# Optimization experiments

Hardware: AMD Instinct MI355X
Metric: run time of the kernel (lower is better)

The kernel has to match this reference:

```python
import jax, jax.numpy as jnp
import numpy as np

N_ITER, N_TAPS, N_DELAY, N_SRC = 2, 4, 1, 4
EPS = 1e-3
TINY = 1e-20
BATCH, N_CHAN, N_FREQ, N_FRAMES = 2, 6, 320, 500


def mag_sq(x):
    return x.real ** 2 + x.imag ** 2


def divide(num, denom, eps):
    return num / jnp.maximum(denom, eps)


def make_xbar(X, n_taps, n_delay):
    # X: (..., c, f, n) -> X_bar: (..., c, f, t, n); tap t is X delayed by n_delay + t
    n = X.shape[-1]
    pad = [(0, 0)] * (X.ndim - 1)
    taps = [jnp.pad(X, pad + [(n_delay + t, 0)])[..., :n] for t in range(n_taps)]
    return jnp.stack(taps, axis=-2)


def background_update(W, H, C_XX, C_XbarX, eps=1e-5):
    # recompute J from W, H and input covariances (ridge-loaded solve)
    n_src = W.shape[-3]
    A1 = jnp.einsum('...sfc,...cfd->...fsd', W, C_XX)
    A2 = jnp.einsum('...sfdt,...dtfc->...fsc', H, C_XbarX)
    Am = A1 + A2
    mat = Am[..., :n_src]
    load = jnp.abs(jnp.diagonal(mat, axis1=-2, axis2=-1)).sum(axis=-1)[..., None, None]
    load = jnp.maximum(load * eps, eps) * jnp.eye(n_src, dtype=mat.dtype)
    load = jax.lax.stop_gradient(load)
    J_H = jnp.linalg.solve(mat + load, Am[..., n_src:])
    return jnp.moveaxis(J_H.conj(), -1, -3)  # (..., n_bak, f, n_src)


def iss_type1(src, Y, w, eps):
    n = Y.shape[-1]
    Ys = Y[..., src, :, :]
    vn = jnp.einsum('...cfn,...cfn,...fn->...cf', w, Y, Ys.conj()) / n
    vd = jnp.einsum('...cfn,...fn->...cf', w, mag_sq(Ys)) / n
    v = divide(vn, vd, eps)
    vs = 1.0 - 1.0 / jnp.sqrt(jnp.maximum(vd[..., src, :], eps))
    return v.at[..., src, :].set(vs.astype(v.dtype))


def iss_type2(Y, Zs, w, eps):
    vn = jnp.einsum('...cfn,...cfn,...fn->...cf', w, Y, Zs.conj())
    vd = jnp.einsum('...cfn,...fn->...cf', w, mag_sq(Zs))
    return divide(vn, vd, eps)


def iss_type3(src, tap, Y, X_bar, w, eps):
    Xst = X_bar[..., src, :, tap, :]
    vn = jnp.einsum('...cfn,...cfn,...fn->...cf', w, Y, Xst.conj())
    vd = jnp.einsum('...cfn,...fn->...cf', w, mag_sq(Xst))
    return divide(vn, vd, eps)


def mat_up1(W, H, A, v, src, eps):
    Wn = W - jnp.einsum('...cf,...fd->...cfd', v, W[..., src, :, :])
    Hn = H - jnp.einsum('...cf,...fdt->...cfdt', v, H[..., src, :, :, :])
    u = jnp.einsum('...sfc,...cf->...sf', A[..., :v.shape[-2]], v)
    u = u / (1.0 - v[..., src:src + 1, :] + eps)
    return Wn, Hn, A.at[..., src].add(u)


def mat_up2(W, J, A, v, g, eps):
    n_src = W.shape[-3]
    v2 = v[..., :n_src, :] + jnp.einsum('...sfc,...cf->...sf', W[..., n_src:], v[..., n_src:, :])
    W1 = W[..., :n_src] - jnp.einsum('...cf,...fd->...cfd', v[..., :n_src, :], g)
    Wn = jnp.concatenate([W1, W[..., n_src:]], axis=-1)
    Jn = J - jnp.einsum('...cf,...fd->...cfd', v[..., n_src:, :], g)
    Av = jnp.einsum('...sfc,...cf->...sf', A[..., :v2.shape[-2]], v2)
    gA = jnp.einsum('...fs,...sfc->...fc', g, A[..., :g.shape[-1], :, :])
    denom = 1.0 - jnp.einsum('...cf,...fc->...f', v2, gA)
    mul = denom.conj() / (mag_sq(denom) + eps)
    An = A + jnp.einsum('...sf,...fc->...sfc', Av, gA * mul[..., None])
    return Wn, Jn, An


def bak_update_vector(p, d, g, eps):
    gdg = jnp.sum(mag_sq(g) / (d + eps), axis=-2)
    gdp = jnp.sum(g.conj() * p / (d + eps), axis=-2)
    b = 1.0 - gdp
    b1 = mag_sq(b)
    a = b1 * gdg + TINY
    beta = (-b1 + jnp.sqrt(b1 ** 2 + 4.0 * a)) / (2.0 * a)
    ell1 = beta * b
    ell2 = (1.0 / jnp.sqrt(eps + gdg)).astype(ell1.dtype)
    ell = jnp.where(b1 > eps ** 2, ell1, ell2)
    return (p - ell[..., None, :] * g) / (d + eps)


def bak_update(bak, Y, Z, X, W, J, A, w, eps):
    n_src, n_freq, n_frames = Y.shape[-3:]
    n_chan = X.shape[-3]
    Zs = Z[..., bak, :, :] + X[..., n_src + bak, :, :]
    norm = 1.0 / n_frames
    ones = jnp.ones(w.shape[:-3] + (n_chan - n_src, n_freq, n_frames), w.dtype)
    wz = jnp.concatenate([w, ones], axis=-3)
    YZ = jnp.concatenate([Y, Z], axis=-3)
    p = jnp.einsum('...cfn,...cfn,...fn->...cf', YZ, wz, Zs.conj()) * norm
    d = jnp.einsum('...cfn,...fn->...cf', wz, mag_sq(Zs)) * norm
    A2 = jnp.concatenate([A, jnp.einsum('...sfc,...cfd->...sfd', A, W[..., n_src:])], axis=-1)
    g = jnp.einsum('...fs,...sfc->...cf', J[..., bak, :, :], A2).conj()
    v = bak_update_vector(p, d, g, eps)
    YZ = YZ - jnp.einsum('...cf,...fn->...cfn', v, Zs)
    return v, YZ[..., :n_src, :, :], YZ[..., n_src:, :, :]


def iss_updates(Y, X, X_bar, W, H, A, w, J, Z, eps):
    n_src = Y.shape[-3]
    n_chan = X.shape[-3]
    n_taps = X_bar.shape[-2]
    n_bak = n_chan - n_src
    # 1) background rows (structured type-2 updates)
    for bak in range(n_bak):
        v, Y, Z = bak_update(bak, Y, Z, X, W, J, A, w, eps)
        g = J[..., bak, :, :]
        W, J, A = mat_up2(W, J, A, v, g, eps)
    # 2) source directions (type 1)
    for src in range(n_src):
        v = iss_type1(src, Y, w, eps)
        Y = Y - jnp.einsum('...cf,...fn->...cfn', v, Y[..., src, :, :])
        W, H, A = mat_up1(W, H, A, v, src, eps)
    # 3) background directions (type 2)
    for bak in range(n_bak):
        v = iss_type2(Y, Z[..., bak, :, :], w, eps)
        Y = Y - jnp.einsum('...cf,...fn->...cfn', v, Z[..., bak, :, :])
        W = W.at[..., :n_src].add(-jnp.einsum('...cf,...fd->...cfd', v, J[..., bak, :, :]))
        W = W.at[..., n_src + bak].add(v)
    if n_bak > 0:
        # keep A consistent: A = inv(W1 + W2 J) per frequency
        Binv = W[..., :n_src] + jnp.einsum('...sfc,...cfd->...sfd', W[..., n_src:], J)
        A = jnp.moveaxis(jnp.linalg.inv(jnp.moveaxis(Binv, -2, -3)), -3, -2)
    # 4) dereverberation taps (type 3)
    for src in range(n_chan):
        for tap in range(n_taps):
            v = iss_type3(src, tap, Y, X_bar, w, eps)
            Y = Y - jnp.einsum('...cf,...fn->...cfn', v, X_bar[..., src, :, tap, :])
            H = H.at[..., src, tap].add(v)
    return Y, Z, W, H, J, A


def _forward(X):
    batch = X.shape[:-3]
    n_chan, n_freq, n_frames = X.shape[-3:]
    n_src = N_SRC
    X_bar = make_xbar(X, N_TAPS, N_DELAY)
    W = jnp.broadcast_to(jnp.eye(n_src, n_chan, dtype=X.dtype)[:, None, :], batch + (n_src, n_freq, n_chan))
    H = jnp.zeros(batch + (n_src, n_freq, n_chan, N_TAPS), X.dtype)
    A = jnp.broadcast_to(jnp.eye(n_src, dtype=X.dtype)[:, None, :], batch + (n_src, n_freq, n_src))
    # initialize background demixing J from input second-order statistics
    C_XX = jnp.einsum('...cfn,...dfn->...cfd', X, X.conj()) / n_frames
    C_XbarX = jnp.einsum('...dftn,...cfn->...dtfc', X_bar, X.conj()) / n_frames
    J = background_update(W, H, C_XX, C_XbarX)
    Y = X[..., :n_src, :, :]
    Z = jnp.einsum('...cfd,...dfn->...cfn', J, X[..., :n_src, :, :]) - X[..., n_src:, :, :]
    for _ in range(N_ITER):
        # Gauss (time-varying) source-model weights, shared across frequencies
        w = 1.0 / jnp.maximum(jnp.mean(mag_sq(Y), axis=-2, keepdims=True), EPS)
        w = jnp.broadcast_to(w, Y.shape)
        Y, Z, W, H, J, A = iss_updates(Y, X, X_bar, W, H, A, w, J, Z, EPS)
    return Y


def setup_inputs():
    key = jax.random.key(0)
    k1, k2 = jax.random.split(key)
    shape = (BATCH, N_CHAN, N_FREQ, N_FRAMES)
    return {"X_real": jax.random.normal(k1, shape, jnp.float32),
            "X_imag": jax.random.normal(k2, shape, jnp.float32)}


def reference(X_real, X_imag):
    X = jax.lax.complex(X_real, X_imag)
    return _forward(X)
```

## Files before the change

kernel.cpp:

```cpp
#include <hip/hip_runtime.h>

#define NFR 500
#define NFQ 320
#define NB  2
#define NC  6
#define NS  4
#define NBK 2
#define NT  4
#define NDLY 1
#define EPSF 1e-3f
#define TINYF 1e-20f

#define NP   512
#define XPAD 8
#define XLEN (XPAD + NP)
#define NCH  8
#define FPC  (NFQ / NCH)

typedef float f2 __attribute__((ext_vector_type(2)));

__device__ __forceinline__ f2 mk2(float r, float i){ f2 t; t.x = r; t.y = i; return t; }
__device__ __forceinline__ f2 cmul(f2 a, f2 b){ return a.xx*b + a.yy*mk2(-b.y, b.x); }
__device__ __forceinline__ f2 cmulc(f2 a, f2 b){ return b.xx*a + b.yy*mk2(a.y, -a.x); }
__device__ __forceinline__ f2 conjc(f2 a){ return mk2(a.x, -a.y); }
__device__ __forceinline__ float cmag2(f2 a){ return a.x*a.x + a.y*a.y; }
__device__ __forceinline__ f2 cinv(f2 a){ float m = a.x*a.x + a.y*a.y; return mk2(a.x/m, -a.y/m); }

#define DPPF(x, ctrl) __int_as_float(__builtin_amdgcn_mov_dpp(__float_as_int(x), (ctrl), 0xF, 0xF, true))
__device__ __forceinline__ float wred64(float x){
  x += DPPF(x, 0x111);
  x += DPPF(x, 0x112);
  x += DPPF(x, 0x114);
  x += DPPF(x, 0x118);
  x += DPPF(x, 0x142);
  x += DPPF(x, 0x143);
  return __int_as_float(__builtin_amdgcn_readlane(__float_as_int(x), 63));
}

__global__ __launch_bounds__(512) void k_wpartX(const float* __restrict__ Xr,
                                                const float* __restrict__ Xi,
                                                float* __restrict__ wacc)
{
  const int bs = blockIdx.x / NCH;
  const int ch = blockIdx.x % NCH;
  const int n  = threadIdx.x;
  if (n >= NFR) return;
  const int b = bs / NS, s = bs % NS;
  const size_t rowb = ((size_t)(b*NC + s)*NFQ)*NFR;
  float acc = 0.f;
  for (int ff = 0; ff < FPC; ++ff) {
    size_t idx = rowb + (size_t)(ch*FPC + ff)*NFR + n;
    float xr = Xr[idx], xi = Xi[idx];
    acc += xr*xr + xi*xi;
  }
  wacc[((size_t)(ch*NB*NS + bs))*NFR + n] = acc;
}

__global__ __launch_bounds__(512) void k_wpart(const f2* __restrict__ Yg,
                                               float* __restrict__ wacc)
{
  const int bs = blockIdx.x / NCH;
  const int ch = blockIdx.x % NCH;
  const int n  = threadIdx.x;
  if (n >= NFR) return;
  const f2* row = Yg + (size_t)bs*NFQ*NFR;
  f2 acc2 = mk2(0.f,0.f);
  for (int ff = 0; ff < FPC; ++ff) {
    f2 y = row[(size_t)(ch*FPC + ff)*NFR + n];
    acc2 += y*y;
  }
  wacc[((size_t)(ch*NB*NS + bs))*NFR + n] = acc2.x + acc2.y;
}

__global__ __launch_bounds__(256, 3) void k_iter(
  const float* __restrict__ Xr, const float* __restrict__ Xi,
  f2* __restrict__ Yg, f2* __restrict__ Zg,
  f2* __restrict__ Wg, f2* __restrict__ Jg, f2* __restrict__ Ag,
  const float* __restrict__ wacc, float* __restrict__ outR,
  const int first, const int last)
{
  __shared__ f2 sXp[NC][XLEN];
  __shared__ f2 sZ[NBK][NP];
  __shared__ f2 sS[NP];
  __shared__ f2 sW[NS][NC];
  __shared__ f2 sJ[NBK][NS];
  __shared__ f2 sA[NS][NS];
  __shared__ f2 sB[NS][2*NS];
  __shared__ f2 sv[NC], sg[NC], sgo[NS];
  __shared__ float sd[NC];
  __shared__ f2 sp[NC];
  __shared__ f2 sAv[NS], sgA[NS], sWsrc[NC];

  const int bf = blockIdx.x;
  const int b = bf / NFQ, f = bf % NFQ;
  const int tid = threadIdx.x, wv = tid >> 6, lane = tid & 63;

  f2 yreg[8];
  float wreg[8];

  for (int c = 0; c < NC; ++c) {
    const size_t base = ((size_t)(b*NC + c)*NFQ + f)*NFR;
    for (int j = tid; j < XLEN; j += 256) {
      int n = j - XPAD;
      sXp[c][j] = (n >= 0 && n < NFR) ? mk2(Xr[base+n], Xi[base+n]) : mk2(0.f,0.f);
    }
  }

  if (first) {
    __syncthreads();
    for (int p = wv; p < NS*NC; p += 4) {
      int s = p / NC, d = p % NC;
      f2 ar2 = mk2(0.f,0.f), ai2 = mk2(0.f,0.f);
#pragma unroll
      for (int i = 0; i < 8; ++i) {
        int n = lane + 64*i;
        f2 xs = sXp[s][XPAD+n], xd = sXp[d][XPAD+n];
        ar2 += xs * xd;
        ai2 += xs.yx * mk2(xd.x, -xd.y);
      }
      float ar = wred64(ar2.x + ar2.y), ai = wred64(ai2.x + ai2.y);
      if (lane == 0) sB[s][d] = mk2(ar*(1.f/NFR), ai*(1.f/NFR));
    }
    if (tid >= 192 && tid < 192 + NS*NC) {
      int t = tid - 192; sW[t/NC][t%NC] = (t/NC == t%NC) ? mk2(1.f,0.f) : mk2(0.f,0.f);
    } else if (tid >= 224 && tid < 224 + NS*NS) {
      int t = tid - 224; sA[t/NS][t%NS] = (t/NS == t%NS) ? mk2(1.f,0.f) : mk2(0.f,0.f);
    }
    __syncthreads();
    if (tid == 0) {
      f2 M[NS][NC];
      for (int s = 0; s < NS; ++s)
        for (int d = 0; d < NC; ++d) M[s][d] = sB[s][d];
      float dsum = 0.f;
      for (int s = 0; s < NS; ++s) dsum += sqrtf(cmag2(M[s][s]));
      float load = fmaxf(dsum*1e-5f, 1e-5f);
      for (int s = 0; s < NS; ++s) M[s][s].x += load;
      for (int col = 0; col < NS; ++col) {
        int piv = col; float best = cmag2(M[col][col]);
        for (int r = col+1; r < NS; ++r) { float m = cmag2(M[r][col]); if (m > best){best=m; piv=r;} }
        if (piv != col) for (int k = 0; k < NC; ++k) { f2 t=M[col][k]; M[col][k]=M[piv][k]; M[piv][k]=t; }
        f2 ip = cinv(M[col][col]);
        for (int k = col; k < NC; ++k) M[col][k] = cmul(M[col][k], ip);
        for (int r = 0; r < NS; ++r) if (r != col) {
          f2 fac = M[r][col];
          for (int k = col; k < NC; ++k) M[r][k] -= cmul(fac, M[col][k]);
        }
      }
      for (int k = 0; k < NBK; ++k)
        for (int s = 0; s < NS; ++s) sJ[k][s] = conjc(M[s][NS+k]);
    }
    __syncthreads();
    for (int n = tid; n < NP; n += 256) {
      f2 x0 = sXp[0][XPAD+n], x1 = sXp[1][XPAD+n], x2 = sXp[2][XPAD+n], x3 = sXp[3][XPAD+n];
      f2 a0 = -sXp[NS+0][XPAD+n];
      a0 += cmul(sJ[0][0], x0); a0 += cmul(sJ[0][1], x1);
      a0 += cmul(sJ[0][2], x2); a0 += cmul(sJ[0][3], x3);
      f2 a1 = -sXp[NS+1][XPAD+n];
      a1 += cmul(sJ[1][0], x0); a1 += cmul(sJ[1][1], x1);
      a1 += cmul(sJ[1][2], x2); a1 += cmul(sJ[1][3], x3);
      sZ[0][n] = a0; sZ[1][n] = a1;
    }
    {
      const int bs = b*NS + wv;
#pragma unroll
      for (int i = 0; i < 8; ++i) {
        int n = lane + 64*i;
        yreg[i] = sXp[wv][XPAD+n];
        if (n < NFR) {
          float a = 0.f;
#pragma unroll
          for (int cc = 0; cc < NCH; ++cc) a += wacc[((size_t)(cc*NB*NS + bs))*NFR + n];
          wreg[i] = 1.0f / fmaxf(a * (1.0f/(float)NFQ), EPSF);
        } else wreg[i] = 0.f;
      }
    }
    __syncthreads();
  } else {
    for (int k = 0; k < NBK; ++k) {
      const size_t zb = ((size_t)(b*NBK + k)*NFQ + f)*NFR;
      for (int n = tid; n < NP; n += 256) sZ[k][n] = (n < NFR) ? Zg[zb+n] : mk2(0.f,0.f);
    }
    {
      const size_t yb = ((size_t)(b*NS + wv)*NFQ + f)*NFR;
      const int bs = b*NS + wv;
#pragma unroll
      for (int i = 0; i < 8; ++i) {
        int n = lane + 64*i;
        if (n < NFR) {
          yreg[i] = Yg[yb+n];
          float a = 0.f;
#pragma unroll
          for (int cc = 0; cc < NCH; ++cc) a += wacc[((size_t)(cc*NB*NS + bs))*NFR + n];
          wreg[i] = 1.0f / fmaxf(a * (1.0f/(float)NFQ), EPSF);
        } else { yreg[i] = mk2(0.f,0.f); wreg[i] = 0.f; }
      }
    }
    if (tid < NS*NC) sW[tid/NC][tid%NC] = Wg[((size_t)(b*NS + tid/NC)*NFQ + f)*NC + tid%NC];
    else if (tid < NS*NC + NBK*NS) { int t=tid-NS*NC; sJ[t/NS][t%NS] = Jg[((size_t)(b*NBK+t/NS)*NFQ+f)*NS + t%NS]; }
    else if (tid < NS*NC + NBK*NS + NS*NS) { int t=tid-NS*NC-NBK*NS; sA[t/NS][t%NS] = Ag[((size_t)(b*NS+t/NS)*NFQ+f)*NS + t%NS]; }
    __syncthreads();
  }

  f2 vloc[NC];

  for (int bak = 0; bak < NBK; ++bak) {
    if (bak > 0 && tid < 16) {
      int s = tid >> 2, c = tid & 3;
      f2 v2[NS];
#pragma unroll
      for (int t = 0; t < NS; ++t)
        v2[t] = vloc[t] + cmul(sW[t][NS+0], vloc[NS+0]) + cmul(sW[t][NS+1], vloc[NS+1]);
      f2 den = mk2(1.f,0.f);
#pragma unroll
      for (int cc = 0; cc < NS; ++cc) den -= cmul(v2[cc], sgA[cc]);
      float m2 = cmag2(den) + EPSF;
      f2 mul = mk2(den.x/m2, -den.y/m2);
      sA[s][c] += cmul(sAv[s], cmul(sgA[c], mul));
    }
    __syncthreads();

    f2 zs[8];
    {
      f2 pr2 = mk2(0.f,0.f), pi2 = mk2(0.f,0.f), dd2 = mk2(0.f,0.f);
#pragma unroll
      for (int i = 0; i < 8; ++i) {
        int n = lane+64*i;
        zs[i] = sZ[bak][n] + sXp[NS+bak][XPAD+n];
        f2 wy = wreg[i]*yreg[i];
        pr2 += wy * zs[i];
        pi2 += wy.yx * mk2(zs[i].x, -zs[i].y);
        dd2 += (wreg[i]*zs[i]) * zs[i];
      }
      float pr = wred64(pr2.x+pr2.y), pi = wred64(pi2.x+pi2.y), dd = wred64(dd2.x+dd2.y);
      if (lane == 0) { sp[wv] = mk2(pr*(1.f/NFR), pi*(1.f/NFR)); sd[wv] = dd*(1.f/NFR); }
      if (wv < NBK) {
        f2 qr2 = mk2(0.f,0.f), qi2 = mk2(0.f,0.f), qd2 = mk2(0.f,0.f);
#pragma unroll
        for (int i = 0; i < 8; ++i) {
          f2 y = sZ[wv][lane+64*i];
          qr2 += y * zs[i];
          qi2 += y.yx * mk2(zs[i].x, -zs[i].y);
          qd2 += zs[i]*zs[i];
        }
        float qr = wred64(qr2.x+qr2.y), qi = wred64(qi2.x+qi2.y), qd = wred64(qd2.x+qd2.y);
        if (lane == 0) { sp[NS+wv] = mk2(qr*(1.f/NFR), qi*(1.f/NFR)); sd[NS+wv] = qd*(1.f/NFR); }
      }
    }
    if (tid < NC) {
      int c = tid; f2 acc = mk2(0.f,0.f);
      for (int s = 0; s < NS; ++s) {
        f2 a2;
        if (c < NS) a2 = sA[s][c];
        else {
          a2 = mk2(0.f,0.f);
          for (int k = 0; k < NS; ++k) a2 += cmul(sA[s][k], sW[k][c]);
        }
        acc += cmul(sJ[bak][s], a2);
      }
      sg[c] = conjc(acc);
    } else if (tid >= 8 && tid < 8+NS) {
      sgo[tid-8] = sJ[bak][tid-8];
    }
    __syncthreads();

    {
      float gdg = 0.f; f2 gdp = mk2(0.f,0.f);
#pragma unroll
      for (int c = 0; c < NC; ++c) {
        f2 gc = sg[c]; float id = 1.0f/(sd[c] + EPSF);
        gdg += cmag2(gc) * id;
        gdp += id * cmulc(sp[c], gc);
      }
      f2 bb = mk2(1.0f - gdp.x, -gdp.y);
      float b1 = cmag2(bb);
      float a = b1*gdg + TINYF;
      float beta = (-b1 + sqrtf(b1*b1 + 4.0f*a)) / (2.0f*a);
      f2 ell = (b1 > EPSF*EPSF) ? (beta*bb) : mk2(1.0f/sqrtf(EPSF + gdg), 0.f);
#pragma unroll
      for (int c = 0; c < NC; ++c)
        vloc[c] = (1.0f/(sd[c] + EPSF)) * (sp[c] - cmul(ell, sg[c]));
    }
    {
      f2 vc = vloc[wv];
#pragma unroll
      for (int i = 0; i < 8; ++i) yreg[i] -= cmul(vc, zs[i]);
      if (wv < NBK) {
        f2 v2c = vloc[NS+wv];
#pragma unroll
        for (int i = 0; i < 8; ++i) sZ[wv][lane+64*i] -= cmul(v2c, zs[i]);
      }
    }
    __syncthreads();

    if (tid < NS) {
      f2 v2[NS];
#pragma unroll
      for (int t = 0; t < NS; ++t)
        v2[t] = vloc[t] + cmul(sW[t][NS+0], vloc[NS+0]) + cmul(sW[t][NS+1], vloc[NS+1]);
      f2 acc = mk2(0.f,0.f);
#pragma unroll
      for (int c = 0; c < NS; ++c) acc += cmul(sA[tid][c], v2[c]);
      sAv[tid] = acc;
    } else if (tid < 2*NS) {
      int c = tid - NS; f2 acc = mk2(0.f,0.f);
#pragma unroll
      for (int s = 0; s < NS; ++s) acc += cmul(sgo[s], sA[s][c]);
      sgA[c] = acc;
    } else if (tid < 2*NS + 16) {
      int idx = tid - 2*NS; int cc = idx >> 2, d = idx & 3;
      sW[cc][d] -= cmul(vloc[cc], sgo[d]);
    } else if (tid < 2*NS + 16 + 8) {
      int idx = tid - 2*NS - 16; int k = idx >> 2, d = idx & 3;
      sJ[k][d] -= cmul(vloc[NS+k], sgo[d]);
    }
    __syncthreads();
  }

  for (int src = 0; src < NS; ++src) {
    if (wv == src) {
#pragma unroll
      for (int i = 0; i < 8; ++i) sS[lane+64*i] = yreg[i];
    }
    if (tid < NC) sWsrc[tid] = sW[src][tid];
    if (src == 0) {
      if (tid < 16) {
        int s = tid >> 2, c = tid & 3;
        f2 v2[NS];
#pragma unroll
        for (int t = 0; t < NS; ++t)
          v2[t] = vloc[t] + cmul(sW[t][NS+0], vloc[NS+0]) + cmul(sW[t][NS+1], vloc[NS+1]);
        f2 den = mk2(1.f,0.f);
#pragma unroll
        for (int cc = 0; cc < NS; ++cc) den -= cmul(v2[cc], sgA[cc]);
        float m2 = cmag2(den) + EPSF;
        f2 mul = mk2(den.x/m2, -den.y/m2);
        sA[s][c] += cmul(sAv[s], cmul(sgA[c], mul));
      }
    } else if (tid >= 8 && tid < 8+NS) {
      int r = tid - 8, prev = src - 1;
      f2 acc = mk2(0.f,0.f);
#pragma unroll
      for (int c = 0; c < NS; ++c) acc += cmul(sA[r][c], sv[c]);
      float den = 1.0f - sv[prev].x + EPSF;
      sA[r][prev] += (1.0f/den) * acc;
    }
    __syncthreads();

    {
      f2 ys[8];
      f2 nr2 = mk2(0.f,0.f), ni2 = mk2(0.f,0.f), dd2 = mk2(0.f,0.f);
#pragma unroll
      for (int i = 0; i < 8; ++i) {
        ys[i] = sS[lane+64*i];
        f2 wy = wreg[i]*yreg[i];
        nr2 += wy * ys[i];
        ni2 += wy.yx * mk2(ys[i].x, -ys[i].y);
        dd2 += (wreg[i]*ys[i]) * ys[i];
      }
      float nr = wred64(nr2.x+nr2.y)*(1.f/NFR);
      float ni = wred64(ni2.x+ni2.y)*(1.f/NFR);
      float dd = wred64(dd2.x+dd2.y)*(1.f/NFR);
      f2 vc;
      if (wv == src) vc = mk2(1.0f - 1.0f/sqrtf(fmaxf(dd, EPSF)), 0.f);
      else           vc = (1.0f/fmaxf(dd, EPSF)) * mk2(nr, ni);
      if (lane == 0) sv[wv] = vc;
#pragma unroll
      for (int i = 0; i < 8; ++i) yreg[i] -= cmul(vc, ys[i]);
      if (lane < NC) sW[wv][lane] -= cmul(vc, sWsrc[lane]);
    }
    __syncthreads();
  }

  {
    f2 pr0=mk2(0,0), pi0=mk2(0,0), dd0=mk2(0,0);
    f2 pr1=mk2(0,0), pi1=mk2(0,0), dd1=mk2(0,0);
    f2 crr=mk2(0,0), cri=mk2(0,0);
    f2 z0c[8], z1c[8];
#pragma unroll
    for (int i = 0; i < 8; ++i) {
      f2 z0 = sZ[0][lane+64*i], z1 = sZ[1][lane+64*i];
      z0c[i] = z0; z1c[i] = z1;
      f2 wy = wreg[i]*yreg[i];
      f2 wz0 = wreg[i]*z0;
      pr0 += wy * z0;  pi0 += wy.yx * mk2(z0.x, -z0.y);  dd0 += wz0 * z0;
      pr1 += wy * z1;  pi1 += wy.yx * mk2(z1.x, -z1.y);  dd1 += (wreg[i]*z1) * z1;
      crr += wz0 * z1; cri += wz0.yx * mk2(z1.x, -z1.y);
    }
    float P0r = wred64(pr0.x+pr0.y), P0i = wred64(pi0.x+pi0.y), D0 = wred64(dd0.x+dd0.y);
    float P1r = wred64(pr1.x+pr1.y), P1i = wred64(pi1.x+pi1.y), D1 = wred64(dd1.x+dd1.y);
    float Rr  = wred64(crr.x+crr.y), Ri  = wred64(cri.x+cri.y);
    f2 v0 = (1.0f/fmaxf(D0, EPSF)) * mk2(P0r, P0i);
    f2 P1c = mk2(P1r, P1i) - cmul(v0, mk2(Rr, Ri));
    f2 v1 = (1.0f/fmaxf(D1, EPSF)) * P1c;
#pragma unroll
    for (int i = 0; i < 8; ++i) yreg[i] -= cmul(v0, z0c[i]) + cmul(v1, z1c[i]);
    if (lane < NS) sW[wv][lane] -= cmul(v0, sJ[0][lane]) + cmul(v1, sJ[1][lane]);
    else if (lane == NS)   sW[wv][NS+0] += v0;
    else if (lane == NS+1) sW[wv][NS+1] += v1;
  }
  __syncthreads();

  if (!last) {
    if (tid < 16) {
      int s = tid >> 2, d = tid & 3;
      f2 acc = sW[s][d];
      acc += cmul(sW[s][NS+0], sJ[0][d]);
      acc += cmul(sW[s][NS+1], sJ[1][d]);
      sB[s][d] = acc;
      sB[s][NS+d] = (s==d) ? mk2(1.f,0.f) : mk2(0.f,0.f);
    }
    __syncthreads();
    if (tid == 0) {
      for (int col = 0; col < NS; ++col) {
        int piv = col; float best = cmag2(sB[col][col]);
        for (int r = col+1; r < NS; ++r) { float m = cmag2(sB[r][col]); if (m > best) { best = m; piv = r; } }
        if (piv != col) for (int k = 0; k < 2*NS; ++k) { f2 t = sB[col][k]; sB[col][k] = sB[piv][k]; sB[piv][k] = t; }
        f2 ip = cinv(sB[col][col]);
        for (int k = 0; k < 2*NS; ++k) sB[col][k] = cmul(sB[col][k], ip);
        for (int r = 0; r < NS; ++r) if (r != col) {
          f2 fac = sB[r][col];
          for (int k = 0; k < 2*NS; ++k) sB[r][k] -= cmul(fac, sB[col][k]);
        }
      }
    }
  }

  {
#pragma unroll 1
    for (int src = 0; src < NC; ++src) {
      const f2* __restrict__ xrow = &sXp[src][0];
#pragma unroll
      for (int tap = 0; tap < NT; ++tap) {
        const int xoff = XPAD - (NDLY + tap) + lane;
        f2 xs[8];
        f2 nr2 = mk2(0.f,0.f), ni2 = mk2(0.f,0.f), dd2 = mk2(0.f,0.f);
#pragma unroll
        for (int i = 0; i < 8; ++i) {
          xs[i] = xrow[xoff + 64*i];
          f2 wy = wreg[i]*yreg[i];
          nr2 += wy * xs[i];
          ni2 += wy.yx * mk2(xs[i].x, -xs[i].y);
          dd2 += (wreg[i]*xs[i]) * xs[i];
        }
        float nr = wred64(nr2.x+nr2.y), ni = wred64(ni2.x+ni2.y), dd = wred64(dd2.x+dd2.y);
        f2 vc = (1.0f/fmaxf(dd, EPSF)) * mk2(nr, ni);
#pragma unroll
        for (int i = 0; i < 8; ++i) yreg[i] -= cmul(vc, xs[i]);
      }
    }
  }

  {
    const size_t yb = ((size_t)(b*NS + wv)*NFQ + f)*NFR;
    if (last) {
#pragma unroll
      for (int i = 0; i < 8; ++i) { int n = lane+64*i; if (n < NFR) outR[yb+n] = yreg[i].x; }
    } else {
#pragma unroll
      for (int i = 0; i < 8; ++i) { int n = lane+64*i; if (n < NFR) Yg[yb+n] = yreg[i]; }
    }
  }
  if (!last) {
    __syncthreads();
    for (int k = 0; k < NBK; ++k) {
      const size_t zb = ((size_t)(b*NBK+k)*NFQ + f)*NFR;
      for (int n = tid; n < NFR; n += 256) Zg[zb+n] = sZ[k][n];
    }
    if (tid < NS*NC) Wg[((size_t)(b*NS + tid/NC)*NFQ + f)*NC + tid%NC] = sW[tid/NC][tid%NC];
    else if (tid < NS*NC + NBK*NS) { int t = tid - NS*NC; Jg[((size_t)(b*NBK + t/NS)*NFQ + f)*NS + t%NS] = sJ[t/NS][t%NS]; }
    else if (tid < NS*NC + NBK*NS + NS*NS) { int t = tid - NS*NC - NBK*NS; Ag[((size_t)(b*NS + t/NS)*NFQ + f)*NS + t%NS] = sB[t/NS][NS + t%NS]; }
  }
}

extern "C" void kernel_launch(void* const* d_in, const int* in_sizes, int n_in,
                              void* d_out, int out_size, void* d_ws, size_t ws_size,
                              hipStream_t stream)
{
  (void)in_sizes; (void)n_in; (void)out_size; (void)ws_size;
  const float* Xr = (const float*)d_in[0];
  const float* Xi = (const float*)d_in[1];
  float* outR = (float*)d_out;

  char* ws = (char*)d_ws;
  size_t off = 0;
  f2* Yg = (f2*)(ws + off); off += (size_t)NB*NS*NFQ*NFR*sizeof(f2);
  f2* Zg = (f2*)(ws + off); off += (size_t)NB*NBK*NFQ*NFR*sizeof(f2);
  f2* Wg = (f2*)(ws + off); off += (size_t)NB*NS*NFQ*NC*sizeof(f2);
  f2* Jg = (f2*)(ws + off); off += (size_t)NB*NBK*NFQ*NS*sizeof(f2);
  f2* Ag = (f2*)(ws + off); off += (size_t)NB*NS*NFQ*NS*sizeof(f2);
  float* wacc = (float*)(ws + off); off += (size_t)NCH*NB*NS*NFR*sizeof(float);

  k_wpartX<<<NB*NS*NCH, 512, 0, stream>>>(Xr, Xi, wacc);
  k_iter<<<NB*NFQ, 256, 0, stream>>>(Xr, Xi, Yg, Zg, Wg, Jg, Ag, wacc, outR, 1, 0);
  k_wpart<<<NB*NS*NCH, 512, 0, stream>>>(Yg, wacc);
  k_iter<<<NB*NFQ, 256, 0, stream>>>(Xr, Xi, Yg, Zg, Wg, Jg, Ag, wacc, outR, 0, 1);
}
```

Before: 114.4 us.

## Compute source weights in one block per source and scalarize per-thread vectors

The weight-reduction kernels now use one block per (batch, source) that loops over all frequencies with four accumulators and writes the final weight directly. Previously eight chunk partials were written and k_iter summed them for every block. The Gaussian-elimination solve now works in place on shared memory instead of a local array, and the per-thread vloc array is replaced by six scalar registers so it cannot spill to scratch memory. The cost is that the reduction grid drops from 64 blocks to 8, leaving most CUs idle and making each thread read 320 rows serially.

```diff
diff --git a/kernel.cpp b/kernel.cpp
--- a/kernel.cpp
+++ b/kernel.cpp
@@ -14,8 +14,6 @@
 #define NP   512
 #define XPAD 8
 #define XLEN (XPAD + NP)
-#define NCH  8
-#define FPC  (NFQ / NCH)
 
 typedef float f2 __attribute__((ext_vector_type(2)));
 
@@ -37,46 +35,54 @@
   return __int_as_float(__builtin_amdgcn_readlane(__float_as_int(x), 63));
 }
 
-__global__ __launch_bounds__(512) void k_wpartX(const float* __restrict__ Xr,
-                                                const float* __restrict__ Xi,
-                                                float* __restrict__ wacc)
+__global__ __launch_bounds__(512) void k_wX(const float* __restrict__ Xr,
+                                            const float* __restrict__ Xi,
+                                            float* __restrict__ wg)
 {
-  const int bs = blockIdx.x / NCH;
-  const int ch = blockIdx.x % NCH;
+  const int bs = blockIdx.x;
   const int n  = threadIdx.x;
   if (n >= NFR) return;
   const int b = bs / NS, s = bs % NS;
-  const size_t rowb = ((size_t)(b*NC + s)*NFQ)*NFR;
-  float acc = 0.f;
-  for (int ff = 0; ff < FPC; ++ff) {
-    size_t idx = rowb + (size_t)(ch*FPC + ff)*NFR + n;
-    float xr = Xr[idx], xi = Xi[idx];
-    acc += xr*xr + xi*xi;
-  }
-  wacc[((size_t)(ch*NB*NS + bs))*NFR + n] = acc;
+  const size_t rowb = ((size_t)(b*NC + s)*NFQ)*NFR + n;
+  float a0 = 0.f, a1 = 0.f, a2 = 0.f, a3 = 0.f;
+#pragma unroll 4
+  for (int f = 0; f < NFQ; f += 4) {
+    float r0 = Xr[rowb + (size_t)(f+0)*NFR], i0 = Xi[rowb + (size_t)(f+0)*NFR];
+    float r1 = Xr[rowb + (size_t)(f+1)*NFR], i1 = Xi[rowb + (size_t)(f+1)*NFR];
+    float r2 = Xr[rowb + (size_t)(f+2)*NFR], i2 = Xi[rowb + (size_t)(f+2)*NFR];
+    float r3 = Xr[rowb + (size_t)(f+3)*NFR], i3 = Xi[rowb + (size_t)(f+3)*NFR];
+    a0 += r0*r0 + i0*i0;  a1 += r1*r1 + i1*i1;
+    a2 += r2*r2 + i2*i2;  a3 += r3*r3 + i3*i3;
+  }
+  float acc = (a0 + a1) + (a2 + a3);
+  wg[bs*NFR + n] = 1.0f / fmaxf(acc * (1.0f/(float)NFQ), EPSF);
 }
 
-__global__ __launch_bounds__(512) void k_wpart(const f2* __restrict__ Yg,
-                                               float* __restrict__ wacc)
+__global__ __launch_bounds__(512) void k_wY(const f2* __restrict__ Yg,
+                                            float* __restrict__ wg)
 {
-  const int bs = blockIdx.x / NCH;
-  const int ch = blockIdx.x % NCH;
+  const int bs = blockIdx.x;
   const int n  = threadIdx.x;
   if (n >= NFR) return;
-  const f2* row = Yg + (size_t)bs*NFQ*NFR;
-  f2 acc2 = mk2(0.f,0.f);
-  for (int ff = 0; ff < FPC; ++ff) {
-    f2 y = row[(size_t)(ch*FPC + ff)*NFR + n];
-    acc2 += y*y;
-  }
-  wacc[((size_t)(ch*NB*NS + bs))*NFR + n] = acc2.x + acc2.y;
+  const f2* row = Yg + (size_t)bs*NFQ*NFR + n;
+  f2 a0 = mk2(0.f,0.f), a1 = mk2(0.f,0.f), a2 = mk2(0.f,0.f), a3 = mk2(0.f,0.f);
+#pragma unroll 4
+  for (int f = 0; f < NFQ; f += 4) {
+    f2 y0 = row[(size_t)(f+0)*NFR];
+    f2 y1 = row[(size_t)(f+1)*NFR];
+    f2 y2 = row[(size_t)(f+2)*NFR];
+    f2 y3 = row[(size_t)(f+3)*NFR];
+    a0 += y0*y0; a1 += y1*y1; a2 += y2*y2; a3 += y3*y3;
+  }
+  f2 s2 = (a0 + a1) + (a2 + a3);
+  wg[bs*NFR + n] = 1.0f / fmaxf((s2.x + s2.y) * (1.0f/(float)NFQ), EPSF);
 }
 
 __global__ __launch_bounds__(256, 3) void k_iter(
   const float* __restrict__ Xr, const float* __restrict__ Xi,
   f2* __restrict__ Yg, f2* __restrict__ Zg,
   f2* __restrict__ Wg, f2* __restrict__ Jg, f2* __restrict__ Ag,
-  const float* __restrict__ wacc, float* __restrict__ outR,
+  const float* __restrict__ wg, float* __restrict__ outR,
   const int first, const int last)
 {
   __shared__ f2 sXp[NC][XLEN];
@@ -128,26 +134,23 @@
     }
     __syncthreads();
     if (tid == 0) {
-      f2 M[NS][NC];
-      for (int s = 0; s < NS; ++s)
-        for (int d = 0; d < NC; ++d) M[s][d] = sB[s][d];
       float dsum = 0.f;
-      for (int s = 0; s < NS; ++s) dsum += sqrtf(cmag2(M[s][s]));
+      for (int s = 0; s < NS; ++s) dsum += sqrtf(cmag2(sB[s][s]));
       float load = fmaxf(dsum*1e-5f, 1e-5f);
-      for (int s = 0; s < NS; ++s) M[s][s].x += load;
+      for (int s = 0; s < NS; ++s) sB[s][s].x += load;
       for (int col = 0; col < NS; ++col) {
-        int piv = col; float best = cmag2(M[col][col]);
-        for (int r = col+1; r < NS; ++r) { float m = cmag2(M[r][col]); if (m > best){best=m; piv=r;} }
-        if (piv != col) for (int k = 0; k < NC; ++k) { f2 t=M[col][k]; M[col][k]=M[piv][k]; M[piv][k]=t; }
-        f2 ip = cinv(M[col][col]);
-        for (int k = col; k < NC; ++k) M[col][k] = cmul(M[col][k], ip);
+        int piv = col; float best = cmag2(sB[col][col]);
+        for (int r = col+1; r < NS; ++r) { float m = cmag2(sB[r][col]); if (m > best){best=m; piv=r;} }
+        if (piv != col) for (int k = col; k < NC; ++k) { f2 t=sB[col][k]; sB[col][k]=sB[piv][k]; sB[piv][k]=t; }
+        f2 ip = cinv(sB[col][col]);
+        for (int k = col; k < NC; ++k) sB[col][k] = cmul(sB[col][k], ip);
         for (int r = 0; r < NS; ++r) if (r != col) {
-          f2 fac = M[r][col];
-          for (int k = col; k < NC; ++k) M[r][k] -= cmul(fac, M[col][k]);
+          f2 fac = sB[r][col];
+          for (int k = col; k < NC; ++k) sB[r][k] -= cmul(fac, sB[col][k]);
         }
       }
       for (int k = 0; k < NBK; ++k)
-        for (int s = 0; s < NS; ++s) sJ[k][s] = conjc(M[s][NS+k]);
+        for (int s = 0; s < NS; ++s) sJ[k][s] = conjc(sB[s][NS+k]);
     }
     __syncthreads();
     for (int n = tid; n < NP; n += 256) {
@@ -166,12 +169,7 @@
       for (int i = 0; i < 8; ++i) {
         int n = lane + 64*i;
         yreg[i] = sXp[wv][XPAD+n];
-        if (n < NFR) {
-          float a = 0.f;
-#pragma unroll
-          for (int cc = 0; cc < NCH; ++cc) a += wacc[((size_t)(cc*NB*NS + bs))*NFR + n];
-          wreg[i] = 1.0f / fmaxf(a * (1.0f/(float)NFQ), EPSF);
-        } else wreg[i] = 0.f;
+        wreg[i] = (n < NFR) ? wg[bs*NFR + n] : 0.f;
       }
     }
     __syncthreads();
@@ -186,13 +184,8 @@
 #pragma unroll
       for (int i = 0; i < 8; ++i) {
         int n = lane + 64*i;
-        if (n < NFR) {
-          yreg[i] = Yg[yb+n];
-          float a = 0.f;
-#pragma unroll
-          for (int cc = 0; cc < NCH; ++cc) a += wacc[((size_t)(cc*NB*NS + bs))*NFR + n];
-          wreg[i] = 1.0f / fmaxf(a * (1.0f/(float)NFQ), EPSF);
-        } else { yreg[i] = mk2(0.f,0.f); wreg[i] = 0.f; }
+        if (n < NFR) { yreg[i] = Yg[yb+n]; wreg[i] = wg[bs*NFR + n]; }
+        else         { yreg[i] = mk2(0.f,0.f); wreg[i] = 0.f; }
       }
     }
     if (tid < NS*NC) sW[tid/NC][tid%NC] = Wg[((size_t)(b*NS + tid/NC)*NFQ + f)*NC + tid%NC];
@@ -201,18 +194,17 @@
     __syncthreads();
   }
 
-  f2 vloc[NC];
+  f2 vl0 = mk2(0.f,0.f), vl1 = mk2(0.f,0.f), vl2 = mk2(0.f,0.f);
+  f2 vl3 = mk2(0.f,0.f), vl4 = mk2(0.f,0.f), vl5 = mk2(0.f,0.f);
+#define V2T(t) (vl##t + cmul(sW[t][NS+0], vl4) + cmul(sW[t][NS+1], vl5))
 
   for (int bak = 0; bak < NBK; ++bak) {
     if (bak > 0 && tid < 16) {
       int s = tid >> 2, c = tid & 3;
-      f2 v2[NS];
-#pragma unroll
-      for (int t = 0; t < NS; ++t)
-        v2[t] = vloc[t] + cmul(sW[t][NS+0], vloc[NS+0]) + cmul(sW[t][NS+1], vloc[NS+1]);
+      f2 v20 = V2T(0), v21 = V2T(1), v22 = V2T(2), v23 = V2T(3);
       f2 den = mk2(1.f,0.f);
-#pragma unroll
-      for (int cc = 0; cc < NS; ++cc) den -= cmul(v2[cc], sgA[cc]);
+      den -= cmul(v20, sgA[0]); den -= cmul(v21, sgA[1]);
+      den -= cmul(v22, sgA[2]); den -= cmul(v23, sgA[3]);
       float m2 = cmag2(den) + EPSF;
       f2 mul = mk2(den.x/m2, -den.y/m2);
       sA[s][c] += cmul(sAv[s], cmul(sgA[c], mul));
@@ -276,16 +268,17 @@
       float a = b1*gdg + TINYF;
       float beta = (-b1 + sqrtf(b1*b1 + 4.0f*a)) / (2.0f*a);
       f2 ell = (b1 > EPSF*EPSF) ? (beta*bb) : mk2(1.0f/sqrtf(EPSF + gdg), 0.f);
-#pragma unroll
-      for (int c = 0; c < NC; ++c)
-        vloc[c] = (1.0f/(sd[c] + EPSF)) * (sp[c] - cmul(ell, sg[c]));
-    }
-    {
-      f2 vc = vloc[wv];
+#define CALCV(c) ((1.0f/(sd[c] + EPSF)) * (sp[c] - cmul(ell, sg[c])))
+      vl0 = CALCV(0); vl1 = CALCV(1); vl2 = CALCV(2);
+      vl3 = CALCV(3); vl4 = CALCV(4); vl5 = CALCV(5);
+#undef CALCV
+    }
+    {
+      f2 vc  = (wv == 0) ? vl0 : (wv == 1) ? vl1 : (wv == 2) ? vl2 : vl3;
 #pragma unroll
       for (int i = 0; i < 8; ++i) yreg[i] -= cmul(vc, zs[i]);
       if (wv < NBK) {
-        f2 v2c = vloc[NS+wv];
+        f2 v2c = (wv == 0) ? vl4 : vl5;
 #pragma unroll
         for (int i = 0; i < 8; ++i) sZ[wv][lane+64*i] -= cmul(v2c, zs[i]);
       }
@@ -293,13 +286,11 @@
     __syncthreads();
 
     if (tid < NS) {
-      f2 v2[NS];
-#pragma unroll
-      for (int t = 0; t < NS; ++t)
-        v2[t] = vloc[t] + cmul(sW[t][NS+0], vloc[NS+0]) + cmul(sW[t][NS+1], vloc[NS+1]);
-      f2 acc = mk2(0.f,0.f);
-#pragma unroll
-      for (int c = 0; c < NS; ++c) acc += cmul(sA[tid][c], v2[c]);
+      f2 v20 = V2T(0), v21 = V2T(1), v22 = V2T(2), v23 = V2T(3);
+      f2 acc = cmul(sA[tid][0], v20);
+      acc += cmul(sA[tid][1], v21);
+      acc += cmul(sA[tid][2], v22);
+      acc += cmul(sA[tid][3], v23);
       sAv[tid] = acc;
     } else if (tid < 2*NS) {
       int c = tid - NS; f2 acc = mk2(0.f,0.f);
@@ -308,10 +299,12 @@
       sgA[c] = acc;
     } else if (tid < 2*NS + 16) {
       int idx = tid - 2*NS; int cc = idx >> 2, d = idx & 3;
-      sW[cc][d] -= cmul(vloc[cc], sgo[d]);
+      f2 vcc = (cc == 0) ? vl0 : (cc == 1) ? vl1 : (cc == 2) ? vl2 : vl3;
+      sW[cc][d] -= cmul(vcc, sgo[d]);
     } else if (tid < 2*NS + 16 + 8) {
       int idx = tid - 2*NS - 16; int k = idx >> 2, d = idx & 3;
-      sJ[k][d] -= cmul(vloc[NS+k], sgo[d]);
+      f2 vk = (k == 0) ? vl4 : vl5;
+      sJ[k][d] -= cmul(vk, sgo[d]);
     }
     __syncthreads();
   }
@@ -325,13 +318,10 @@
     if (src == 0) {
       if (tid < 16) {
         int s = tid >> 2, c = tid & 3;
-        f2 v2[NS];
-#pragma unroll
-        for (int t = 0; t < NS; ++t)
-          v2[t] = vloc[t] + cmul(sW[t][NS+0], vloc[NS+0]) + cmul(sW[t][NS+1], vloc[NS+1]);
+        f2 v20 = V2T(0), v21 = V2T(1), v22 = V2T(2), v23 = V2T(3);
         f2 den = mk2(1.f,0.f);
-#pragma unroll
-        for (int cc = 0; cc < NS; ++cc) den -= cmul(v2[cc], sgA[cc]);
+        den -= cmul(v20, sgA[0]); den -= cmul(v21, sgA[1]);
+        den -= cmul(v22, sgA[2]); den -= cmul(v23, sgA[3]);
         float m2 = cmag2(den) + EPSF;
         f2 mul = mk2(den.x/m2, -den.y/m2);
         sA[s][c] += cmul(sAv[s], cmul(sgA[c], mul));
@@ -470,6 +460,7 @@
     else if (tid < NS*NC + NBK*NS) { int t = tid - NS*NC; Jg[((size_t)(b*NBK + t/NS)*NFQ + f)*NS + t%NS] = sJ[t/NS][t%NS]; }
     else if (tid < NS*NC + NBK*NS + NS*NS) { int t = tid - NS*NC - NBK*NS; Ag[((size_t)(b*NS + t/NS)*NFQ + f)*NS + t%NS] = sB[t/NS][NS + t%NS]; }
   }
+#undef V2T
 }
 
 extern "C" void kernel_launch(void* const* d_in, const int* in_sizes, int n_in,
@@ -488,10 +479,10 @@
   f2* Wg = (f2*)(ws + off); off += (size_t)NB*NS*NFQ*NC*sizeof(f2);
   f2* Jg = (f2*)(ws + off); off += (size_t)NB*NBK*NFQ*NS*sizeof(f2);
   f2* Ag = (f2*)(ws + off); off += (size_t)NB*NS*NFQ*NS*sizeof(f2);
-  float* wacc = (float*)(ws + off); off += (size_t)NCH*NB*NS*NFR*sizeof(float);
-
-  k_wpartX<<<NB*NS*NCH, 512, 0, stream>>>(Xr, Xi, wacc);
-  k_iter<<<NB*NFQ, 256, 0, stream>>>(Xr, Xi, Yg, Zg, Wg, Jg, Ag, wacc, outR, 1, 0);
-  k_wpart<<<NB*NS*NCH, 512, 0, stream>>>(Yg, wacc);
-  k_iter<<<NB*NFQ, 256, 0, stream>>>(Xr, Xi, Yg, Zg, Wg, Jg, Ag, wacc, outR, 0, 1);
+  float* wg = (float*)(ws + off); off += (size_t)NB*NS*NFR*sizeof(float);
+
+  k_wX<<<NB*NS, 512, 0, stream>>>(Xr, Xi, wg);
+  k_iter<<<NB*NFQ, 256, 0, stream>>>(Xr, Xi, Yg, Zg, Wg, Jg, Ag, wg, outR, 1, 0);
+  k_wY<<<NB*NS, 512, 0, stream>>>(Yg, wg);
+  k_iter<<<NB*NFQ, 256, 0, stream>>>(Xr, Xi, Yg, Zg, Wg, Jg, Ag, wg, outR, 0, 1);
 }
```

New measurement: 136.7 us. 19.4% more time.
